# Kernel tuning notes

Measured on AMD Instinct MI355X. Metric: run time of the kernel, lower is better.

## Reference

```python
import jax, jax.numpy as jnp
import numpy as np

N = 8192       # nodes
E = 262144     # edges per graph view (avg degree 32)
D_IN = 200     # input feature dim
D = 100        # hidden dim
H = 2          # GAT heads (concat=False -> mean over heads)
K = 25         # nearest_neighbor in DHGLayer
A_H = 50       # Attention module hidden dim
LRELU = 0.2
BN_EPS = 1e-5


def _bn_eval(x, gamma, beta):
    # BatchNorm1d in eval mode with running_mean=0, running_var=1 (as initialized)
    return x * (gamma / jnp.sqrt(1.0 + BN_EPS)) + beta


def _gat(x, src, dst, W, att_src, att_dst, bias):
    # PyG GATConv: heads=H, concat=False (head mean), self-loops added, eval (no dropout)
    n = x.shape[0]
    xp = (x @ W).reshape(n, H, D)                          # (n, H, D)
    loop = jnp.arange(n, dtype=src.dtype)
    s = jnp.concatenate([src, loop])
    d = jnp.concatenate([dst, loop])
    a_s = jnp.einsum('nhc,hc->nh', xp, att_src)
    a_d = jnp.einsum('nhc,hc->nh', xp, att_dst)
    e = jax.nn.leaky_relu(a_s[s] + a_d[d], LRELU)          # (E+n, H)
    m = jax.ops.segment_max(e, d, num_segments=n)
    w = jnp.exp(e - m[d])
    z = jax.ops.segment_sum(w, d, num_segments=n)
    alpha = w / z[d]
    out = jax.ops.segment_sum(alpha[:, :, None] * xp[s], d, num_segments=n)
    return out.mean(axis=1) + bias                          # (n, D)


def _dhg(x, Wkk, bkk, w1, b1, fcW, fcb):
    # DHGLayer at ite=1: only the kNN hyperedge branch is active
    # (wu_knn=1 <= ite < wu_kmeans=2 = wu_struct=2). EdgeConv over a single
    # hyperedge degenerates to identity (softmax over one element).
    nrm = jnp.maximum(jnp.linalg.norm(x, axis=1, keepdims=True), 1e-12)
    xn = x / nrm
    sim = jax.lax.stop_gradient(xn @ xn.T)                 # cosine sim, used only for topk indices
    _, idx = jax.lax.top_k(sim, K)                         # (n, K)
    region = x[idx]                                        # (n, K, D) gather
    # Transform: grouped Conv1d(K, K*K, D) -> per-node KxK mixing weights -> softmax -> mix
    mult = jax.nn.softmax(jnp.einsum('nkd,kjd->nkj', region, Wkk) + bkk, axis=-1)
    tf = jnp.einsum('nkj,njd->nkd', mult, region)          # (n, K, D)
    pooled = jnp.einsum('nkd,k->nd', tf, w1) + b1          # Conv1d(K, 1, 1) pooling
    return jax.nn.relu(pooled @ fcW + fcb)                 # GraphConvolution fc + ReLU


def _atten(x, W1, b1, g, b, W2, b2):
    h = jax.nn.sigmoid(_bn_eval(x @ W1 + b1, g, b))
    return h @ W2 + b2                                     # (n, 1)


def _encoder(inputx, edge_index, fea_edge_index,
             g1_W, g1_as, g1_ad, g1_b, g2_W, g2_as, g2_ad, g2_b,
             g3_W, g3_as, g3_ad, g3_b, g4_W, g4_as, g4_ad, g4_b,
             bn_g, bn_b, bn1_g, bn1_b,
             d1_Wkk, d1_bkk, d1_w1, d1_b1, d1_fcW, d1_fcb,
             d2_Wkk, d2_bkk, d2_w1, d2_b1, d2_fcW, d2_fcb,
             a1_W1, a1_b1, a1_g, a1_bb, a1_W2, a1_b2,
             a2_W1, a2_b1, a2_g, a2_bb, a2_W2, a2_b2):
    fs, fd = fea_edge_index[0], fea_edge_index[1]
    es, ed = edge_index[0], edge_index[1]
    feax1 = jax.nn.relu(_bn_eval(_gat(inputx, fs, fd, g1_W, g1_as, g1_ad, g1_b), bn_g, bn_b))
    x1 = jax.nn.relu(_bn_eval(_gat(inputx, es, ed, g2_W, g2_as, g2_ad, g2_b), bn1_g, bn1_b))
    feax1 = _dhg(feax1, d1_Wkk, d1_bkk, d1_w1, d1_b1, d1_fcW, d1_fcb)
    feax2 = _gat(feax1, fs, fd, g3_W, g3_as, g3_ad, g3_b)
    x1 = _dhg(x1, d2_Wkk, d2_bkk, d2_w1, d2_b1, d2_fcW, d2_fcb)
    x2 = _gat(x1, es, ed, g4_W, g4_as, g4_ad, g4_b)
    att1 = _atten(feax2, a1_W1, a1_b1, a1_g, a1_bb, a1_W2, a1_b2)
    att2 = _atten(x2, a2_W1, a2_b1, a2_g, a2_bb, a2_W2, a2_b2)
    att = jax.nn.softmax(jnp.concatenate([att1, att2], axis=1), axis=1)
    return att[:, :1] * feax2 + att[:, 1:] * x2            # (N, D)


def setup_inputs() -> dict:
    key = jax.random.key(0)
    kit = iter(jax.random.split(key, 64))
    nrm = lambda shape, scale: jax.random.normal(next(kit), shape, dtype=jnp.float32) * scale
    inp = {}
    inp['inputx'] = nrm((N, D_IN), 1.0)
    inp['edge_index'] = jax.random.randint(next(kit), (2, E), 0, N)
    inp['fea_edge_index'] = jax.random.randint(next(kit), (2, E), 0, N)
    inp['edge_list'] = jax.random.randint(next(kit), (N, K), 0, N)  # unused at ite=1
    for name, din in (('g1', D_IN), ('g2', D_IN), ('g3', D), ('g4', D)):
        inp[name + '_W'] = nrm((din, H * D), din ** -0.5)
        inp[name + '_as'] = nrm((H, D), D ** -0.5)
        inp[name + '_ad'] = nrm((H, D), D ** -0.5)
        inp[name + '_b'] = jnp.zeros((D,), jnp.float32)
    inp['bn_g'] = jnp.ones((D,), jnp.float32)
    inp['bn_b'] = jnp.zeros((D,), jnp.float32)
    inp['bn1_g'] = jnp.ones((D,), jnp.float32)
    inp['bn1_b'] = jnp.zeros((D,), jnp.float32)
    for name in ('d1', 'd2'):
        inp[name + '_Wkk'] = nrm((K, K, D), D ** -0.5)
        inp[name + '_bkk'] = jnp.zeros((K, K), jnp.float32)
        inp[name + '_w1'] = nrm((K,), K ** -0.5)
        inp[name + '_b1'] = jnp.zeros((1,), jnp.float32)
        inp[name + '_fcW'] = nrm((D, D), D ** -0.5)
        inp[name + '_fcb'] = jnp.zeros((D,), jnp.float32)
    for name in ('a1', 'a2'):
        inp[name + '_W1'] = nrm((D, A_H), D ** -0.5)
        inp[name + '_b1'] = jnp.zeros((A_H,), jnp.float32)
        inp[name + '_g'] = jnp.ones((A_H,), jnp.float32)
        inp[name + '_bb'] = jnp.zeros((A_H,), jnp.float32)
        inp[name + '_W2'] = nrm((A_H, 1), A_H ** -0.5)
        inp[name + '_b2'] = jnp.zeros((1,), jnp.float32)
    return inp


def reference(inputx, edge_index, fea_edge_index, edge_list,
              g1_W, g1_as, g1_ad, g1_b, g2_W, g2_as, g2_ad, g2_b,
              g3_W, g3_as, g3_ad, g3_b, g4_W, g4_as, g4_ad, g4_b,
              bn_g, bn_b, bn1_g, bn1_b,
              d1_Wkk, d1_bkk, d1_w1, d1_b1, d1_fcW, d1_fcb,
              d2_Wkk, d2_bkk, d2_w1, d2_b1, d2_fcW, d2_fcb,
              a1_W1, a1_b1, a1_g, a1_bb, a1_W2, a1_b2,
              a2_W1, a2_b1, a2_g, a2_bb, a2_W2, a2_b2):
    # edge_list is ignored: structured-neighbor branch is not warmed up at ite=1
    return _encoder(inputx, edge_index, fea_edge_index,
                    g1_W, g1_as, g1_ad, g1_b, g2_W, g2_as, g2_ad, g2_b,
                    g3_W, g3_as, g3_ad, g3_b, g4_W, g4_as, g4_ad, g4_b,
                    bn_g, bn_b, bn1_g, bn1_b,
                    d1_Wkk, d1_bkk, d1_w1, d1_b1, d1_fcW, d1_fcb,
                    d2_Wkk, d2_bkk, d2_w1, d2_b1, d2_fcW, d2_fcb,
                    a1_W1, a1_b1, a1_g, a1_bb, a1_W2, a1_b2,
                    a2_W1, a2_b1, a2_g, a2_bb, a2_W2, a2_b2)
```

## Files before the change

### kernel.cpp

```cpp
#include <hip/hip_runtime.h>
#include <math.h>

#define NN 8192
#define EE 262144
#define KNN 25
#define INIT_COLS 512
#define CAP 512
#define INF INFINITY

typedef unsigned int u32;
typedef unsigned long long u64;

__device__ __forceinline__ float lrelu02(float x){ return x > 0.f ? x : 0.2f*x; }
__device__ __forceinline__ u32 fkey(float f){ u32 b = __float_as_uint(f); return b ^ (u32)(((int)b >> 31) | (int)0x80000000); }

__global__ __launch_bounds__(256) void k_count(const int* __restrict__ dst, int* __restrict__ deg) {
  int e = blockIdx.x*256 + threadIdx.x;
  if (e < EE) atomicAdd(&deg[dst[e]], 1);
}

__global__ __launch_bounds__(1024) void k_scan(const int* __restrict__ deg, int* __restrict__ rowptr) {
  __shared__ int lds[1024];
  int t = threadIdx.x;
  int v[8]; int s = 0;
#pragma unroll
  for (int i=0;i<8;i++){ v[i] = deg[t*8+i]; s += v[i]; }
  lds[t] = s; __syncthreads();
  for (int off=1; off<1024; off<<=1) {
    int x = (t>=off)? lds[t-off] : 0;
    __syncthreads();
    lds[t] += x;
    __syncthreads();
  }
  int base = (t==0)? 0 : lds[t-1];
  if (t==0) rowptr[0] = 0;
  int run = base;
#pragma unroll
  for (int i=0;i<8;i++){ run += v[i]; rowptr[t*8+i+1] = run; }
}

__global__ __launch_bounds__(256) void k_scatter(const int* __restrict__ src, const int* __restrict__ dst,
                          const int* __restrict__ rowptr, int* __restrict__ cursor,
                          int* __restrict__ csr) {
  int e = blockIdx.x*256 + threadIdx.x;
  if (e < EE) {
    int d = dst[e];
    int p = rowptr[d] + atomicAdd(&cursor[d], 1);
    csr[p] = src[e];
  }
}

__global__ __launch_bounds__(256) void k_gemm_small(const float* __restrict__ A, const float* __restrict__ B,
                                                    float* __restrict__ C, int Ncols, int Kdim) {
  __shared__ float Al[50][65];
  __shared__ float Bl[50][65];
  int t = threadIdx.x;
  int tr = t >> 4, tc = t & 15;
  int r0 = blockIdx.x * 64, c0 = blockIdx.y * 64;
  float acc[4][4] = {};
  for (int kc = 0; kc < Kdim; kc += 50) {
    for (int fl = t; fl < 64*50; fl += 256) {
      int m = fl / 50, k = fl - m*50;
      Al[k][m] = A[(long)(r0+m)*Kdim + kc + k];
    }
    for (int fl = t; fl < 50*64; fl += 256) {
      int k = fl >> 6, c = fl & 63;
      int cg = c0 + c;
      Bl[k][c] = (cg < Ncols) ? B[(long)(kc+k)*Ncols + cg] : 0.f;
    }
    __syncthreads();
    for (int k = 0; k < 50; k++) {
      float a_[4], b_[4];
#pragma unroll
      for (int i=0;i<4;i++) a_[i] = Al[k][tr*4+i];
#pragma unroll
      for (int j=0;j<4;j++) b_[j] = Bl[k][tc*4+j];
#pragma unroll
      for (int i=0;i<4;i++)
#pragma unroll
        for (int j=0;j<4;j++) acc[i][j] += a_[i]*b_[j];
    }
    __syncthreads();
  }
#pragma unroll
  for (int i=0;i<4;i++){
    int r = r0 + tr*4 + i;
#pragma unroll
    for (int j=0;j<4;j++){
      int c = c0 + tc*4 + j;
      if (c < Ncols) C[(long)r*Ncols + c] = acc[i][j];
    }
  }
}

__global__ __launch_bounds__(256) void k_gat_coef(const float* __restrict__ xp, const float* __restrict__ as_w,
                                                  const float* __restrict__ ad_w, float* __restrict__ asb,
                                                  float* __restrict__ adb) {
  int g = blockIdx.x*256 + threadIdx.x;
  int n = g >> 2, q = g & 3;
  int h = q >> 1, sd = q & 1;
  const float4* xr = (const float4*)(xp + (long)n*200 + h*100);
  const float4* wr = (const float4*)((sd ? ad_w : as_w) + h*100);
  float acc = 0.f;
#pragma unroll
  for (int q4=0;q4<25;q4++){
    float4 xv = xr[q4], wv = wr[q4];
    acc += xv.x*wv.x + xv.y*wv.y + xv.z*wv.z + xv.w*wv.w;
  }
  (sd ? adb : asb)[n*2 + h] = acc;
}

__global__ __launch_bounds__(256) void k_gat_agg(const float* __restrict__ xp, const float* __restrict__ asb,
                                                 const float* __restrict__ adb, const int* __restrict__ rowptr,
                                                 const int* __restrict__ csr, const float* __restrict__ bias,
                                                 const float* __restrict__ bng, const float* __restrict__ bnb,
                                                 int bnrelu, float* __restrict__ out) {
  __shared__ int esrc[256];
  __shared__ float ew0[256], ew1[256];
  __shared__ float red[2][4];
  __shared__ float ohead[200];
  int i = blockIdx.x, t = threadIdx.x;
  int lane = t & 63, wv = t >> 6;
  int beg = rowptr[i];
  int deg = rowptr[i+1] - beg;
  float ad0 = adb[i*2+0], ad1 = adb[i*2+1];
  float m0 = -INF, m1 = -INF, z0 = 0.f, z1 = 0.f, acc = 0.f;
  int h = (t >= 100) ? 1 : 0;
  int tot = deg + 1;
  for (int base = 0; base < tot; base += 256) {
    int cnt = min(256, tot - base);
    int j = base + t;
    float e0 = -INF, e1 = -INF; int s = i;
    if (t < cnt) {
      if (j < deg) s = csr[beg + j];
      float as0 = asb[s*2+0], as1 = asb[s*2+1];
      e0 = lrelu02(as0 + ad0);
      e1 = lrelu02(as1 + ad1);
    }
    esrc[t] = s;
    float r0v = e0, r1v = e1;
    for (int off=32; off; off>>=1){ r0v = fmaxf(r0v, __shfl_xor(r0v,off)); r1v = fmaxf(r1v, __shfl_xor(r1v,off)); }
    if (lane == 0){ red[0][wv] = r0v; red[1][wv] = r1v; }
    __syncthreads();
    float nm0 = fmaxf(m0, fmaxf(fmaxf(red[0][0],red[0][1]), fmaxf(red[0][2],red[0][3])));
    float nm1 = fmaxf(m1, fmaxf(fmaxf(red[1][0],red[1][1]), fmaxf(red[1][2],red[1][3])));
    float w0 = (t<cnt)? expf(e0-nm0) : 0.f;
    float w1e = (t<cnt)? expf(e1-nm1) : 0.f;
    ew0[t] = w0; ew1[t] = w1e;
    float s0 = w0, s1 = w1e;
    for (int off=32; off; off>>=1){ s0 += __shfl_xor(s0,off); s1 += __shfl_xor(s1,off); }
    __syncthreads();
    if (lane == 0){ red[0][wv] = s0; red[1][wv] = s1; }
    __syncthreads();
    float cs0 = red[0][0]+red[0][1]+red[0][2]+red[0][3];
    float cs1 = red[1][0]+red[1][1]+red[1][2]+red[1][3];
    float rf0 = expf(m0 - nm0);
    float rf1 = expf(m1 - nm1);
    z0 = z0*rf0 + cs0; z1 = z1*rf1 + cs1;
    m0 = nm0; m1 = nm1;
    if (t < 200) {
      acc *= (h==0) ? rf0 : rf1;
      const float* ew = (h==0) ? ew0 : ew1;
      for (int jj = 0; jj < cnt; jj++) {
        acc += ew[jj] * xp[(long)esrc[jj]*200 + t];
      }
    }
    __syncthreads();
  }
  if (t < 200) ohead[t] = acc / ((h==0) ? z0 : z1);
  __syncthreads();
  if (t < 100) {
    float v = 0.5f*(ohead[t] + ohead[100+t]) + bias[t];
    if (bnrelu) {
      v = v * (bng[t]*rsqrtf(1.f+1e-5f)) + bnb[t];
      v = fmaxf(v, 0.f);
    }
    out[(long)i*100 + t] = v;
  }
}

__global__ __launch_bounds__(256) void k_norm(const float* __restrict__ x, float* __restrict__ xn) {
  int w = threadIdx.x >> 6, lane = threadIdx.x & 63;
  long n = blockIdx.x*4 + w;
  float a = x[n*100 + lane];
  float b = (lane < 36) ? x[n*100 + 64 + lane] : 0.f;
  float ss = a*a + b*b;
  for (int off=32; off; off>>=1) ss += __shfl_xor(ss, off);
  float sc = 1.f / fmaxf(sqrtf(ss), 1e-12f);
  xn[n*100 + lane] = a*sc;
  if (lane < 36) xn[n*100 + 64 + lane] = b*sc;
}

__global__ __launch_bounds__(256) void k_sim(const float* __restrict__ xn, float* __restrict__ simbuf,
                                             int cbase, int stripe) {
  __shared__ float Al[50][132];
  __shared__ float Bl[50][132];
  int t = threadIdx.x;
  int tr = t >> 4, tc = t & 15;
  int r0 = blockIdx.x * 128;
  int cb = blockIdx.y * 128;
  float acc[8][8] = {};
  for (int kc = 0; kc < 100; kc += 50) {
    for (int fl = t; fl < 128*50; fl += 256) {
      int m = fl / 50, k = fl - m*50;
      Al[k][m] = xn[(long)(r0+m)*100 + kc + k];
      Bl[k][m] = xn[(long)(cbase+cb+m)*100 + kc + k];
    }
    __syncthreads();
    for (int k = 0; k < 50; k++) {
      float4 a0 = *(const float4*)&Al[k][tr*8];
      float4 a1 = *(const float4*)&Al[k][tr*8+4];
      float4 b0 = *(const float4*)&Bl[k][tc*8];
      float4 b1 = *(const float4*)&Bl[k][tc*8+4];
      float a_[8] = {a0.x,a0.y,a0.z,a0.w,a1.x,a1.y,a1.z,a1.w};
      float b_[8] = {b0.x,b0.y,b0.z,b0.w,b1.x,b1.y,b1.z,b1.w};
#pragma unroll
      for (int i=0;i<8;i++)
#pragma unroll
        for (int j=0;j<8;j++) acc[i][j] += a_[i]*b_[j];
    }
    __syncthreads();
  }
#pragma unroll
  for (int i=0;i<8;i++){
    long r = r0 + tr*8 + i;
    float* crow = simbuf + r*(long)stripe + cb + tc*8;
    float4 o0 = make_float4(acc[i][0],acc[i][1],acc[i][2],acc[i][3]);
    float4 o1 = make_float4(acc[i][4],acc[i][5],acc[i][6],acc[i][7]);
    *(float4*)&crow[0] = o0;
    *(float4*)&crow[4] = o1;
  }
}

__global__ __launch_bounds__(256) void k_sim_f(const float* __restrict__ xn, const u32* __restrict__ thr,
                                               int* __restrict__ cnt, u64* __restrict__ candbuf, int cbase) {
  __shared__ float Al[50][132];
  __shared__ float Bl[50][132];
  int t = threadIdx.x;
  int tr = t >> 4, tc = t & 15;
  int r0 = blockIdx.x * 128;
  int cb = blockIdx.y * 128;
  float acc[8][8] = {};
  for (int kc = 0; kc < 100; kc += 50) {
    for (int fl = t; fl < 128*50; fl += 256) {
      int m = fl / 50, k = fl - m*50;
      Al[k][m] = xn[(long)(r0+m)*100 + kc + k];
      Bl[k][m] = xn[(long)(cbase+cb+m)*100 + kc + k];
    }
    __syncthreads();
    for (int k = 0; k < 50; k++) {
      float4 a0 = *(const float4*)&Al[k][tr*8];
      float4 a1 = *(const float4*)&Al[k][tr*8+4];
      float4 b0 = *(const float4*)&Bl[k][tc*8];
      float4 b1 = *(const float4*)&Bl[k][tc*8+4];
      float a_[8] = {a0.x,a0.y,a0.z,a0.w,a1.x,a1.y,a1.z,a1.w};
      float b_[8] = {b0.x,b0.y,b0.z,b0.w,b1.x,b1.y,b1.z,b1.w};
#pragma unroll
      for (int i=0;i<8;i++)
#pragma unroll
        for (int j=0;j<8;j++) acc[i][j] += a_[i]*b_[j];
    }
    __syncthreads();
  }
#pragma unroll
  for (int i=0;i<8;i++){
    int r = r0 + tr*8 + i;
    u32 T = thr[r];
#pragma unroll
    for (int j=0;j<8;j++){
      u32 key = fkey(acc[i][j]);
      if (key > T) {
        int c = cbase + cb + tc*8 + j;
        int p = atomicAdd(&cnt[r], 1);
        if (p < CAP) candbuf[(long)r*CAP + p] = ((u64)key << 32) | (u32)(0xFFFFFFFFu - (u32)c);
      }
    }
  }
}

__global__ __launch_bounds__(256) void k_topk_sel(const float* __restrict__ simbuf,
                                                  u64* __restrict__ candu, u32* __restrict__ thr) {
  __shared__ int hist[256];
  __shared__ int scr2[2];
  __shared__ int cgt, ceq;
  __shared__ u64 win[32];
  __shared__ u32 tie[INIT_COLS];
  int row = blockIdx.x, t = threadIdx.x, lane = t & 63, w = t >> 6;
  const float* srow = simbuf + (long)row*INIT_COLS;
  u32 kk[2]; int col[2];
  {
    float2 f = *(const float2*)&srow[2*t];
    kk[0] = fkey(f.x); col[0] = 2*t;
    kk[1] = fkey(f.y); col[1] = 2*t+1;
  }
  u32 prefix = 0; int base_gt = 0;
#pragma unroll
  for (int lvl = 0; lvl < 4; lvl++) {
    int shift = 24 - 8*lvl;
    hist[t] = 0;
    if (lvl == 0 && t == 0) { cgt = 0; ceq = 0; }
    __syncthreads();
    u32 mhi = (lvl == 0) ? 0u : (0xFFFFFFFFu << (32 - 8*lvl));
#pragma unroll
    for (int i = 0; i < 2; i++)
      if ((kk[i] & mhi) == (prefix & mhi)) atomicAdd(&hist[(kk[i] >> shift) & 0xFF], 1);
    __syncthreads();
    if (w == 0) {
      int h0 = hist[4*lane], h1 = hist[4*lane+1], h2 = hist[4*lane+2], h3 = hist[4*lane+3];
      int s = h0 + h1 + h2 + h3;
      int acc = s;
      for (int off = 1; off < 64; off <<= 1) {
        int o = __shfl_down(acc, off);
        if (lane + off < 64) acc += o;
      }
      int T = base_gt + (acc - s);
      int b0c = -1; int cumc = T;
      if (cumc < 25 && cumc + h3 >= 25) b0c = 3;
      else { cumc += h3;
        if (cumc < 25 && cumc + h2 >= 25) b0c = 2;
        else { cumc += h2;
          if (cumc < 25 && cumc + h1 >= 25) b0c = 1;
          else { cumc += h1;
            if (cumc < 25 && cumc + h0 >= 25) b0c = 0;
          }
        }
      }
      u64 bal = __ballot(b0c >= 0);
      int ls = __ffsll(bal) - 1;
      int b0 = __shfl(b0c, ls);
      int cum = __shfl(cumc, ls);
      int bl = __shfl(lane, ls);
      if (lane == 0) { scr2[0] = 4*bl + b0; scr2[1] = cum; }
    }
    __syncthreads();
    prefix |= ((u32)scr2[0]) << shift;
    base_gt = scr2[1];
  }
  u32 K25 = prefix;
#pragma unroll
  for (int i = 0; i < 2; i++) {
    if (kk[i] > K25) {
      int p = atomicAdd(&cgt, 1);
      win[p] = ((u64)kk[i] << 32) | (u32)(0xFFFFFFFFu - (u32)col[i]);
    } else if (kk[i] == K25) {
      int p = atomicAdd(&ceq, 1);
      tie[p] = (u32)col[i];
    }
  }
  __syncthreads();
  int wc = cgt, tc = ceq, need = 25 - wc;
  if (tc == need) {
    if (t < need) win[wc + t] = ((u64)K25 << 32) | (u32)(0xFFFFFFFFu - tie[t]);
  } else if (w == 0) {
    for (int sel = 0; sel < need; sel++) {
      u32 m = 0xFFFFFFFFu;
      for (int i = lane; i < tc; i += 64) m = min(m, tie[i]);
      for (int off = 32; off; off >>= 1) m = min(m, (u32)__shfl_xor((int)m, off));
      for (int i = lane; i < tc; i += 64) if (tie[i] == m) tie[i] = 0xFFFFFFFFu;
      if (lane == 0) win[wc + sel] = ((u64)K25 << 32) | (u32)(0xFFFFFFFFu - m);
    }
  }
  __syncthreads();
  if (t < 32) {
    u64 v = (t < 25) ? win[t] : 0ULL;
#pragma unroll
    for (int kb = 2; kb <= 32; kb <<= 1) {
#pragma unroll
      for (int j = kb >> 1; j > 0; j >>= 1) {
        u64 o = __shfl_xor(v, j);
        bool dirAsc = ((t & kb) == 0);
        bool isLow = ((t & j) == 0);
        u64 mn = (v < o) ? v : o;
        u64 mx = (v < o) ? o : v;
        v = (dirAsc == isLow) ? mx : mn;
      }
    }
    if (t < 25) candu[(long)row*25 + t] = v;
  }
  if (t == 0) thr[row] = K25;
}

__global__ __launch_bounds__(256) void k_topk_fmerge(const u64* __restrict__ candu, const int* __restrict__ cnt,
                                                     const u64* __restrict__ candbuf, int* __restrict__ lib) {
  int lane = threadIdx.x & 63;
  int row = blockIdx.x*4 + (threadIdx.x >> 6);
  u64 v = (lane < 25) ? candu[(long)row*25 + lane] : 0ULL;
  int C = cnt[row]; if (C > CAP) C = CAP;
  for (int off = 0; off < C; off += 39) {
    int take = min(39, C - off);
    u64 x = (lane < 25) ? v : ((lane - 25 < take) ? candbuf[(long)row*CAP + off + (lane-25)] : 0ULL);
#pragma unroll
    for (int kb = 2; kb <= 64; kb <<= 1) {
#pragma unroll
      for (int j = kb >> 1; j > 0; j >>= 1) {
        u64 o = __shfl_xor(x, j);
        bool dirAsc = ((lane & kb) == 0);
        bool isLow = ((lane & j) == 0);
        u64 mn = (x < o) ? x : o;
        u64 mx = (x < o) ? o : x;
        x = (dirAsc == isLow) ? mx : mn;
      }
    }
    v = x;
  }
  if (lane < 25) lib[row*KNN + lane] = (int)(0xFFFFFFFFu - (u32)v);
}

__global__ __launch_bounds__(256) void k_dhg_s(const float* __restrict__ x, const int* __restrict__ li,
                                               const float* __restrict__ Wkk, const float* __restrict__ bkk,
                                               const float* __restrict__ w1, float* __restrict__ coefp) {
  __shared__ float Wl[KNN][100];
  __shared__ float bk[KNN];
  __shared__ float w1s;
  int t = threadIdx.x;
  int k = blockIdx.y;
  for (int fl = t; fl < KNN*100; fl += 256) ((float*)Wl)[fl] = Wkk[k*2500 + fl];
  if (t < KNN) bk[t] = bkk[k*KNN + t];
  if (t == 32) w1s = w1[k];
  __syncthreads();
  int n = blockIdx.x*256 + t;
  int id = li[n*KNN + k];
  float4 r4[25];
  const float4* xr = (const float4*)(x + (long)id*100);
#pragma unroll
  for (int q=0;q<25;q++) r4[q] = xr[q];
  float sv[KNN];
  float mx = -INF;
#pragma unroll
  for (int j=0;j<KNN;j++) {
    float acc = bk[j];
#pragma unroll
    for (int q=0;q<25;q++) {
      float4 wvv = *(const float4*)&Wl[j][q*4];
      acc += r4[q].x*wvv.x; acc += r4[q].y*wvv.y; acc += r4[q].z*wvv.z; acc += r4[q].w*wvv.w;
    }
    sv[j] = acc;
    mx = fmaxf(mx, acc);
  }
  float se = 0.f;
#pragma unroll
  for (int j=0;j<KNN;j++){ sv[j] = expf(sv[j]-mx); se += sv[j]; }
  float sc = w1s / se;
#pragma unroll
  for (int j=0;j<KNN;j++) coefp[(long)(k*KNN + j)*NN + n] = sc*sv[j];
}

__global__ __launch_bounds__(256) void k_dhg_reduce(const float* __restrict__ coefp, float* __restrict__ coef) {
  int g = blockIdx.x*256 + threadIdx.x;
  int j = g >> 13;
  int n = g & (NN-1);
  float s = 0.f;
#pragma unroll
  for (int k=0;k<KNN;k++) s += coefp[(long)(k*KNN + j)*NN + n];
  coef[(long)n*KNN + j] = s;
}

__global__ __launch_bounds__(128) void k_dhg_pool(const float* __restrict__ x, const int* __restrict__ li,
                                                  const float* __restrict__ coef, const float* __restrict__ b1,
                                                  const float* __restrict__ fcW, const float* __restrict__ fcb,
                                                  float* __restrict__ out) {
  __shared__ float cf[KNN];
  __shared__ int id[KNN];
  __shared__ float pl[100];
  int n = blockIdx.x; int t = threadIdx.x;
  if (t < KNN) { cf[t] = coef[n*KNN+t]; id[t] = li[n*KNN+t]; }
  __syncthreads();
  if (t < 100) {
    float acc = b1[0];
#pragma unroll
    for (int j=0;j<KNN;j++) acc += cf[j] * x[(long)id[j]*100 + t];
    pl[t] = acc;
  }
  __syncthreads();
  if (t < 100) {
    float o = fcb[t];
    for (int d=0; d<100; d++) o += pl[d] * fcW[d*100 + t];
    out[(long)n*100 + t] = fmaxf(o, 0.f);
  }
}

__global__ __launch_bounds__(128) void k_final(const float* __restrict__ f2b, const float* __restrict__ x2b,
    const float* __restrict__ w1a, const float* __restrict__ b1a, const float* __restrict__ ga, const float* __restrict__ bba,
    const float* __restrict__ w2a, const float* __restrict__ b2a,
    const float* __restrict__ w1b, const float* __restrict__ b1b, const float* __restrict__ gb, const float* __restrict__ bbb,
    const float* __restrict__ w2b, const float* __restrict__ b2b,
    float* __restrict__ outp) {
  __shared__ float f2[100], xr[100], hh[100], att[2];
  int n = blockIdx.x, t = threadIdx.x;
  if (t < 100) { f2[t] = f2b[(long)n*100+t]; xr[t] = x2b[(long)n*100+t]; }
  __syncthreads();
  if (t < 50) {
    float a = b1a[t];
    for (int d=0; d<100; d++) a += f2[d]*w1a[d*50+t];
    a = a*(ga[t]*rsqrtf(1.f+1e-5f)) + bba[t];
    hh[t] = 1.f/(1.f+expf(-a));
  } else if (t >= 64 && t < 114) {
    int jj = t-64;
    float a = b1b[jj];
    for (int d=0; d<100; d++) a += xr[d]*w1b[d*50+jj];
    a = a*(gb[jj]*rsqrtf(1.f+1e-5f)) + bbb[jj];
    hh[50+jj] = 1.f/(1.f+expf(-a));
  }
  __syncthreads();
  {
    int lane = t & 63, w = t >> 6;
    float c = 0.f;
    if (lane < 50) c = hh[w*50 + lane] * (w ? w2b[lane] : w2a[lane]);
    for (int off=32; off; off>>=1) c += __shfl_down(c, off);
    if (lane == 0) att[w] = c + (w ? b2b[0] : b2a[0]);
  }
  __syncthreads();
  if (t < 100) {
    float A1 = att[0], A2 = att[1];
    float mxv = fmaxf(A1, A2);
    float e1 = expf(A1-mxv), e2 = expf(A2-mxv);
    float inv = 1.f/(e1+e2);
    outp[(long)n*100+t] = (e1*inv)*f2[t] + (e2*inv)*xr[t];
  }
}

extern "C" void kernel_launch(void* const* d_in, const int* in_sizes, int n_in,
                              void* d_out, int out_size, void* d_ws, size_t ws_size,
                              hipStream_t stream) {
  (void)in_sizes; (void)n_in; (void)out_size; (void)ws_size;
  const float* inputx = (const float*)d_in[0];
  const int*   ei     = (const int*)d_in[1];
  const int*   fi     = (const int*)d_in[2];
  const float* g1W = (const float*)d_in[4],  *g1as = (const float*)d_in[5],  *g1ad = (const float*)d_in[6],  *g1b = (const float*)d_in[7];
  const float* g2W = (const float*)d_in[8],  *g2as = (const float*)d_in[9],  *g2ad = (const float*)d_in[10], *g2b = (const float*)d_in[11];
  const float* g3W = (const float*)d_in[12], *g3as = (const float*)d_in[13], *g3ad = (const float*)d_in[14], *g3b = (const float*)d_in[15];
  const float* g4W = (const float*)d_in[16], *g4as = (const float*)d_in[17], *g4ad = (const float*)d_in[18], *g4b = (const float*)d_in[19];
  const float* bng = (const float*)d_in[20], *bnb = (const float*)d_in[21];
  const float* bn1g = (const float*)d_in[22], *bn1b = (const float*)d_in[23];
  const float* d1Wkk = (const float*)d_in[24], *d1bkk = (const float*)d_in[25], *d1w1 = (const float*)d_in[26],
             * d1b1 = (const float*)d_in[27], *d1fcW = (const float*)d_in[28], *d1fcb = (const float*)d_in[29];
  const float* d2Wkk = (const float*)d_in[30], *d2bkk = (const float*)d_in[31], *d2w1 = (const float*)d_in[32],
             * d2b1 = (const float*)d_in[33], *d2fcW = (const float*)d_in[34], *d2fcb = (const float*)d_in[35];
  const float* a1W1 = (const float*)d_in[36], *a1b1 = (const float*)d_in[37], *a1g = (const float*)d_in[38],
             * a1bb = (const float*)d_in[39], *a1W2 = (const float*)d_in[40], *a1b2 = (const float*)d_in[41];
  const float* a2W1 = (const float*)d_in[42], *a2b1 = (const float*)d_in[43], *a2g = (const float*)d_in[44],
             * a2bb = (const float*)d_in[45], *a2W2 = (const float*)d_in[46], *a2b2 = (const float*)d_in[47];

  char* wbase = (char*)d_ws; size_t off = 0;
  auto alloc = [&](size_t b)->void*{ off = (off + 255) & ~(size_t)255; void* p = wbase + off; off += b; return p; };
  int* csrEp = (int*)alloc((NN+1)*4);
  int* csrEs = (int*)alloc((size_t)EE*4);
  int* csrFp = (int*)alloc((NN+1)*4);
  int* csrFs = (int*)alloc((size_t)EE*4);
  int* deg   = (int*)alloc(NN*4);
  int* cur   = (int*)alloc(NN*4);
  float* xp    = (float*)alloc((size_t)NN*200*4);
  float* asb   = (float*)alloc((size_t)NN*2*4);
  float* adb   = (float*)alloc((size_t)NN*2*4);
  float* feax1 = (float*)alloc((size_t)NN*100*4);
  float* x1    = (float*)alloc((size_t)NN*100*4);
  float* feax2 = (float*)alloc((size_t)NN*100*4);
  float* x2v   = (float*)alloc((size_t)NN*100*4);
  float* dtmp  = (float*)alloc((size_t)NN*100*4);
  float* xnb   = (float*)alloc((size_t)NN*100*4);
  int*   lib   = (int*)alloc((size_t)NN*KNN*4);
  float* coef  = (float*)alloc((size_t)NN*KNN*4);
  float* simbuf  = (float*)alloc((size_t)NN*INIT_COLS*4);
  u64*   candu   = (u64*)alloc((size_t)NN*KNN*8);
  u32*   thr     = (u32*)alloc((size_t)NN*4);
  int*   cnt     = (int*)alloc((size_t)NN*4);
  u64*   candbuf = (u64*)alloc((size_t)NN*CAP*8);
  float* coefp = simbuf;

  auto buildCSR = [&](const int* e, int* rp, int* cs){
    hipMemsetAsync(deg, 0, NN*4, stream);
    k_count<<<EE/256, 256, 0, stream>>>(e+EE, deg);
    k_scan<<<1, 1024, 0, stream>>>(deg, rp);
    hipMemsetAsync(cur, 0, NN*4, stream);
    k_scatter<<<EE/256, 256, 0, stream>>>(e, e+EE, rp, cur, cs);
  };
  buildCSR(ei, csrEp, csrEs);
  buildCSR(fi, csrFp, csrFs);

  auto GAT = [&](const float* x, int Kdim, const float* W, const float* as_w, const float* ad_w, const float* b,
                 const int* rp, const int* cs, const float* bg, const float* bb, int bnrelu, float* outb){
    k_gemm_small<<<dim3(NN/64, 4), 256, 0, stream>>>(x, W, xp, 200, Kdim);
    k_gat_coef<<<NN*4/256, 256, 0, stream>>>(xp, as_w, ad_w, asb, adb);
    k_gat_agg<<<NN, 256, 0, stream>>>(xp, asb, adb, rp, cs, b, bg, bb, bnrelu, outb);
  };
  auto DHG = [&](const float* x, const float* Wkk, const float* bkk, const float* w1p, const float* b1p,
                 const float* fcW, const float* fcb, float* outb){
    k_norm<<<NN/4, 256, 0, stream>>>(x, xnb);
    k_sim<<<dim3(NN/128, INIT_COLS/128), 256, 0, stream>>>(xnb, simbuf, 0, INIT_COLS);
    k_topk_sel<<<NN, 256, 0, stream>>>(simbuf, candu, thr);
    hipMemsetAsync(cnt, 0, NN*4, stream);
    k_sim_f<<<dim3(NN/128, (NN-INIT_COLS)/128), 256, 0, stream>>>(xnb, thr, cnt, candbuf, INIT_COLS);
    k_topk_fmerge<<<NN/4, 256, 0, stream>>>(candu, cnt, candbuf, lib);
    k_dhg_s<<<dim3(NN/256, KNN), 256, 0, stream>>>(x, lib, Wkk, bkk, w1p, coefp);
    k_dhg_reduce<<<NN*KNN/256, 256, 0, stream>>>(coefp, coef);
    k_dhg_pool<<<NN, 128, 0, stream>>>(x, lib, coef, b1p, fcW, fcb, outb);
  };

  GAT(inputx, 200, g1W, g1as, g1ad, g1b, csrFp, csrFs, bng,  bnb,  1, feax1);
  GAT(inputx, 200, g2W, g2as, g2ad, g2b, csrEp, csrEs, bn1g, bn1b, 1, x1);
  DHG(feax1, d1Wkk, d1bkk, d1w1, d1b1, d1fcW, d1fcb, dtmp);
  GAT(dtmp, 100, g3W, g3as, g3ad, g3b, csrFp, csrFs, nullptr, nullptr, 0, feax2);
  DHG(x1, d2Wkk, d2bkk, d2w1, d2b1, d2fcW, d2fcb, dtmp);
  GAT(dtmp, 100, g4W, g4as, g4ad, g4b, csrEp, csrEs, nullptr, nullptr, 0, x2v);
  k_final<<<NN, 128, 0, stream>>>(feax2, x2v, a1W1, a1b1, a1g, a1bb, a1W2, a1b2,
                                  a2W1, a2b1, a2g, a2bb, a2W2, a2b2, (float*)d_out);
}
```

Before: 1.589 ms.

## Transpose normalized features, aggregate candidate atomics per row, enlarge initial top-k window

k_norm now writes the normalized features transposed (feature-major), so the similarity GEMM tile loads read consecutive nodes instead of strided rows. k_sim_f gathers its above-threshold candidates with a 16-lane prefix sum and issues one atomicAdd per row group instead of one per element. The initial exact top-k stripe grows from 512 to 1024 columns, giving a tighter threshold so fewer candidates pass later, and CAP rises to 768. simbuf, candbuf and coefp now share one workspace region. The risk is that the larger first stripe costs more than the filtering it saves.

```diff
diff --git a/kernel.cpp b/kernel.cpp
--- a/kernel.cpp
+++ b/kernel.cpp
@@ -4,8 +4,8 @@
 #define NN 8192
 #define EE 262144
 #define KNN 25
-#define INIT_COLS 512
-#define CAP 512
+#define INIT_COLS 1024
+#define CAP 768
 #define INF INFINITY
 
 typedef unsigned int u32;
@@ -179,7 +179,7 @@
   }
 }
 
-__global__ __launch_bounds__(256) void k_norm(const float* __restrict__ x, float* __restrict__ xn) {
+__global__ __launch_bounds__(256) void k_norm(const float* __restrict__ x, float* __restrict__ xnT) {
   int w = threadIdx.x >> 6, lane = threadIdx.x & 63;
   long n = blockIdx.x*4 + w;
   float a = x[n*100 + lane];
@@ -187,12 +187,11 @@
   float ss = a*a + b*b;
   for (int off=32; off; off>>=1) ss += __shfl_xor(ss, off);
   float sc = 1.f / fmaxf(sqrtf(ss), 1e-12f);
-  xn[n*100 + lane] = a*sc;
-  if (lane < 36) xn[n*100 + 64 + lane] = b*sc;
-}
-
-__global__ __launch_bounds__(256) void k_sim(const float* __restrict__ xn, float* __restrict__ simbuf,
-                                             int cbase, int stripe) {
+  xnT[(long)lane*NN + n] = a*sc;
+  if (lane < 36) xnT[(long)(64+lane)*NN + n] = b*sc;
+}
+
+__global__ __launch_bounds__(256) void k_sim(const float* __restrict__ xnT, float* __restrict__ simbuf) {
   __shared__ float Al[50][132];
   __shared__ float Bl[50][132];
   int t = threadIdx.x;
@@ -201,10 +200,11 @@
   int cb = blockIdx.y * 128;
   float acc[8][8] = {};
   for (int kc = 0; kc < 100; kc += 50) {
-    for (int fl = t; fl < 128*50; fl += 256) {
-      int m = fl / 50, k = fl - m*50;
-      Al[k][m] = xn[(long)(r0+m)*100 + kc + k];
-      Bl[k][m] = xn[(long)(cbase+cb+m)*100 + kc + k];
+    for (int fl = t; fl < 50*128; fl += 256) {
+      int k = fl >> 7, m = fl & 127;
+      const float* src = xnT + (long)(kc+k)*NN;
+      Al[k][m] = src[r0 + m];
+      Bl[k][m] = src[cb + m];
     }
     __syncthreads();
     for (int k = 0; k < 50; k++) {
@@ -224,7 +224,7 @@
 #pragma unroll
   for (int i=0;i<8;i++){
     long r = r0 + tr*8 + i;
-    float* crow = simbuf + r*(long)stripe + cb + tc*8;
+    float* crow = simbuf + r*(long)INIT_COLS + cb + tc*8;
     float4 o0 = make_float4(acc[i][0],acc[i][1],acc[i][2],acc[i][3]);
     float4 o1 = make_float4(acc[i][4],acc[i][5],acc[i][6],acc[i][7]);
     *(float4*)&crow[0] = o0;
@@ -232,7 +232,7 @@
   }
 }
 
-__global__ __launch_bounds__(256) void k_sim_f(const float* __restrict__ xn, const u32* __restrict__ thr,
+__global__ __launch_bounds__(256) void k_sim_f(const float* __restrict__ xnT, const u32* __restrict__ thr,
                                                int* __restrict__ cnt, u64* __restrict__ candbuf, int cbase) {
   __shared__ float Al[50][132];
   __shared__ float Bl[50][132];
@@ -242,10 +242,11 @@
   int cb = blockIdx.y * 128;
   float acc[8][8] = {};
   for (int kc = 0; kc < 100; kc += 50) {
-    for (int fl = t; fl < 128*50; fl += 256) {
-      int m = fl / 50, k = fl - m*50;
-      Al[k][m] = xn[(long)(r0+m)*100 + kc + k];
-      Bl[k][m] = xn[(long)(cbase+cb+m)*100 + kc + k];
+    for (int fl = t; fl < 50*128; fl += 256) {
+      int k = fl >> 7, m = fl & 127;
+      const float* src = xnT + (long)(kc+k)*NN;
+      Al[k][m] = src[r0 + m];
+      Bl[k][m] = src[cbase + cb + m];
     }
     __syncthreads();
     for (int k = 0; k < 50; k++) {
@@ -262,17 +263,31 @@
     }
     __syncthreads();
   }
+  int sub = t & 15;
 #pragma unroll
   for (int i=0;i<8;i++){
     int r = r0 + tr*8 + i;
     u32 T = thr[r];
-#pragma unroll
-    for (int j=0;j<8;j++){
-      u32 key = fkey(acc[i][j]);
-      if (key > T) {
-        int c = cbase + cb + tc*8 + j;
-        int p = atomicAdd(&cnt[r], 1);
-        if (p < CAP) candbuf[(long)r*CAP + p] = ((u64)key << 32) | (u32)(0xFFFFFFFFu - (u32)c);
+    unsigned m8 = 0;
+#pragma unroll
+    for (int j=0;j<8;j++) if (fkey(acc[i][j]) > T) m8 |= 1u<<j;
+    int c_lane = __popc(m8);
+    int pre = c_lane;
+#pragma unroll
+    for (int off=1; off<16; off<<=1){ int o = __shfl_up(pre, off, 16); if (sub >= off) pre += o; }
+    int tot = __shfl(pre, 15, 16);
+    if (tot > 0){
+      int base = 0;
+      if (sub == 15) base = atomicAdd(&cnt[r], tot);
+      base = __shfl(base, 15, 16);
+      int p = base + pre - c_lane;
+#pragma unroll
+      for (int j=0;j<8;j++) if (m8 & (1u<<j)){
+        if (p < CAP){
+          int c = cbase + cb + tc*8 + j;
+          candbuf[(long)r*CAP + p] = ((u64)fkey(acc[i][j]) << 32) | (u32)(0xFFFFFFFFu - (u32)c);
+        }
+        p++;
       }
     }
   }
@@ -287,11 +302,14 @@
   __shared__ u32 tie[INIT_COLS];
   int row = blockIdx.x, t = threadIdx.x, lane = t & 63, w = t >> 6;
   const float* srow = simbuf + (long)row*INIT_COLS;
-  u32 kk[2]; int col[2];
+  u32 kk[4]; int col[4];
   {
-    float2 f = *(const float2*)&srow[2*t];
-    kk[0] = fkey(f.x); col[0] = 2*t;
-    kk[1] = fkey(f.y); col[1] = 2*t+1;
+    int c0 = 4*t;
+    float4 f = *(const float4*)&srow[c0];
+    kk[0] = fkey(f.x); col[0] = c0;
+    kk[1] = fkey(f.y); col[1] = c0+1;
+    kk[2] = fkey(f.z); col[2] = c0+2;
+    kk[3] = fkey(f.w); col[3] = c0+3;
   }
   u32 prefix = 0; int base_gt = 0;
 #pragma unroll
@@ -302,7 +320,7 @@
     __syncthreads();
     u32 mhi = (lvl == 0) ? 0u : (0xFFFFFFFFu << (32 - 8*lvl));
 #pragma unroll
-    for (int i = 0; i < 2; i++)
+    for (int i = 0; i < 4; i++)
       if ((kk[i] & mhi) == (prefix & mhi)) atomicAdd(&hist[(kk[i] >> shift) & 0xFF], 1);
     __syncthreads();
     if (w == 0) {
@@ -338,7 +356,7 @@
   }
   u32 K25 = prefix;
 #pragma unroll
-  for (int i = 0; i < 2; i++) {
+  for (int i = 0; i < 4; i++) {
     if (kk[i] > K25) {
       int p = atomicAdd(&cgt, 1);
       win[p] = ((u64)kk[i] << 32) | (u32)(0xFFFFFFFFu - (u32)col[i]);
@@ -557,15 +575,17 @@
   float* feax2 = (float*)alloc((size_t)NN*100*4);
   float* x2v   = (float*)alloc((size_t)NN*100*4);
   float* dtmp  = (float*)alloc((size_t)NN*100*4);
-  float* xnb   = (float*)alloc((size_t)NN*100*4);
+  float* xnT   = (float*)alloc((size_t)NN*100*4);
   int*   lib   = (int*)alloc((size_t)NN*KNN*4);
   float* coef  = (float*)alloc((size_t)NN*KNN*4);
-  float* simbuf  = (float*)alloc((size_t)NN*INIT_COLS*4);
-  u64*   candu   = (u64*)alloc((size_t)NN*KNN*8);
-  u32*   thr     = (u32*)alloc((size_t)NN*4);
-  int*   cnt     = (int*)alloc((size_t)NN*4);
-  u64*   candbuf = (u64*)alloc((size_t)NN*CAP*8);
-  float* coefp = simbuf;
+  u64*   candu = (u64*)alloc((size_t)NN*KNN*8);
+  u32*   thr   = (u32*)alloc((size_t)NN*4);
+  int*   cnt   = (int*)alloc((size_t)NN*4);
+  size_t ubytes = (size_t)NN*CAP*8;
+  char* uregion = (char*)alloc(ubytes);
+  float* simbuf  = (float*)uregion;
+  u64*   candbuf = (u64*)uregion;
+  float* coefp   = (float*)uregion;
 
   auto buildCSR = [&](const int* e, int* rp, int* cs){
     hipMemsetAsync(deg, 0, NN*4, stream);
@@ -585,11 +605,11 @@
   };
   auto DHG = [&](const float* x, const float* Wkk, const float* bkk, const float* w1p, const float* b1p,
                  const float* fcW, const float* fcb, float* outb){
-    k_norm<<<NN/4, 256, 0, stream>>>(x, xnb);
-    k_sim<<<dim3(NN/128, INIT_COLS/128), 256, 0, stream>>>(xnb, simbuf, 0, INIT_COLS);
+    k_norm<<<NN/4, 256, 0, stream>>>(x, xnT);
+    k_sim<<<dim3(NN/128, INIT_COLS/128), 256, 0, stream>>>(xnT, simbuf);
     k_topk_sel<<<NN, 256, 0, stream>>>(simbuf, candu, thr);
     hipMemsetAsync(cnt, 0, NN*4, stream);
-    k_sim_f<<<dim3(NN/128, (NN-INIT_COLS)/128), 256, 0, stream>>>(xnb, thr, cnt, candbuf, INIT_COLS);
+    k_sim_f<<<dim3(NN/128, (NN-INIT_COLS)/128), 256, 0, stream>>>(xnT, thr, cnt, candbuf, INIT_COLS);
     k_topk_fmerge<<<NN/4, 256, 0, stream>>>(candu, cnt, candbuf, lib);
     k_dhg_s<<<dim3(NN/256, KNN), 256, 0, stream>>>(x, lib, Wkk, bkk, w1p, coefp);
     k_dhg_reduce<<<NN*KNN/256, 256, 0, stream>>>(coefp, coef);
```

Result: faster. 1.286 ms (-19.1%).
